# Kernel optimization log

Hardware: AMD Instinct MI355X
Metric: run time of the kernel (lower is better)

## Reference

```python
import jax, jax.numpy as jnp
import numpy as np

L, P = 16384, 512
DT_MIN, DT_MAX = 0.001, 0.1
THRESHOLD = 1.0  # spike threshold assumed for cartesian_spike


def setup_inputs() -> dict:
    key = jax.random.key(0)
    k1, k2, k3, k4, k5, k6 = jax.random.split(key, 6)
    u = jax.random.normal(k1, (L, P), dtype=jnp.float32)
    # Stored Lambda param: [..., 0] = log(-Re(Lambda)) with Re(Lambda) < 0, [..., 1] = Im(Lambda)
    lam_real_neg = jax.random.uniform(k2, (P,), minval=0.1, maxval=1.0)  # -Re(Lambda)
    lam_imag = jax.random.normal(k3, (P,)) * 3.0
    Lambda = jnp.stack([jnp.log(lam_real_neg), lam_imag], axis=-1).astype(jnp.float32)
    # init_log_steps: log(dt) uniform in [log(dt_min), log(dt_max)], shape (P, 1)
    log_step = (np.log(DT_MIN) + jax.random.uniform(k4, (P, 1)) * (np.log(DT_MAX) - np.log(DT_MIN))).astype(jnp.float32)
    V_re = jax.random.normal(k5, (P, P), dtype=jnp.float32) / np.sqrt(P)
    V_im = jax.random.normal(k6, (P, P), dtype=jnp.float32) / np.sqrt(P)
    return {"u": u, "Lambda": Lambda, "log_step": log_step, "V_re": V_re, "V_im": V_im}


def _binop(q_i, q_j):
    A_i, b_i = q_i
    A_j, b_j = q_j
    return (A_j * A_i, A_j * b_i + b_j)


def reference(u, Lambda, log_step, V_re, V_im):
    # keep_imag = False: u stays real. discretization = 'zoh', activation = 'cartesian_spike'.
    Lambda_tilde = -jnp.exp(Lambda[..., 0]) + 1j * Lambda[..., 1]            # (P,) complex
    step = jnp.exp(log_step[:, 0])                                            # (P,)
    Lambda_bar = jnp.exp(Lambda_tilde * step)                                 # (P,) |.|<1
    # B_tilde = I, so zoh gives B_bar = diag((Lambda_bar - 1)/Lambda); B_bar @ u_t = coef * u_t
    B_coef = (Lambda_bar - 1.0) / Lambda_tilde                                # (P,)
    Lambda_elements = jnp.broadcast_to(Lambda_bar, (u.shape[0], Lambda_bar.shape[0]))
    Bu_elements = B_coef[None, :] * u.astype(Lambda_bar.dtype)                # (L, P) complex
    _, xs = jax.lax.associative_scan(_binop, (Lambda_elements, Bu_elements))  # (L, P)
    V = V_re + 1j * V_im
    xs = xs @ V.T                                                             # vmap(V @ x) over L
    spikes = (xs.real > THRESHOLD).astype(jnp.float32)                        # cartesian_spike
    return spikes
```

## Files before the change

### kernel.cpp

```cpp
#include <hip/hip_runtime.h>

#define L_LEN   16384
#define P_DIM   512
#define CHUNK   32
#define NCHUNK  512

#define KDIM    1024
#define NDIM    512
#define BM      128
#define BN      64
#define BK      64

typedef __bf16 bf16_t;
typedef __bf16 bf16x8 __attribute__((ext_vector_type(8)));
typedef float  floatx4 __attribute__((ext_vector_type(4)));

__device__ __forceinline__ uint32_t pack_bf16(float a, float b) {
    bf16_t ha = (bf16_t)a, hb = (bf16_t)b;
    return (uint32_t)__builtin_bit_cast(unsigned short, ha)
         | ((uint32_t)__builtin_bit_cast(unsigned short, hb) << 16);
}

__device__ __forceinline__ void ch_consts(float lam0, float lam1, float ls,
                                          float& ar, float& ai,
                                          float& br, float& bi) {
    float lr = -expf(lam0);
    float li = lam1;
    float s  = expf(ls);
    float er = expf(lr * s);
    ar = er * cosf(li * s);
    ai = er * sinf(li * s);
    float dr = ar - 1.0f, di = ai;
    float inv = 1.0f / (lr * lr + li * li);
    br = (dr * lr + di * li) * inv;
    bi = (di * lr - dr * li) * inv;
}

__global__ void __launch_bounds__(256) k_scan_ends(const float* __restrict__ u,
        const float* __restrict__ Lam, const float* __restrict__ lstep,
        const float* __restrict__ Vre, const float* __restrict__ Vim,
        float2* __restrict__ endv, bf16_t* __restrict__ Bt) {
    const int t = threadIdx.x;
    const int c = blockIdx.x;

    {
        int idx = c * 256 + t;
        float2 vr = ((const float2*)Vre)[idx];
        float2 vi = ((const float2*)Vim)[idx];
        ((uint2*)Bt)[idx] = make_uint2(pack_bf16(vr.x, -vi.x),
                                       pack_bf16(vr.y, -vi.y));
    }

    float4 lam4 = ((const float4*)Lam)[t];
    float2 ls2  = ((const float2*)lstep)[t];
    float ar0, ai0, br0, bi0, ar1, ai1, br1, bi1;
    ch_consts(lam4.x, lam4.y, ls2.x, ar0, ai0, br0, bi0);
    ch_consts(lam4.z, lam4.w, ls2.y, ar1, ai1, br1, bi1);

    float xr0 = 0.f, xi0 = 0.f, xr1 = 0.f, xi1 = 0.f;
    const float2* up = (const float2*)(u + (size_t)c * CHUNK * P_DIM) + t;
    #pragma unroll 8
    for (int k = 0; k < CHUNK; ++k) {
        float2 uv = up[(size_t)k * (P_DIM / 2)];
        float nr0 = ar0 * xr0 - ai0 * xi0 + br0 * uv.x;
        float ni0 = ar0 * xi0 + ai0 * xr0 + bi0 * uv.x;
        float nr1 = ar1 * xr1 - ai1 * xi1 + br1 * uv.y;
        float ni1 = ar1 * xi1 + ai1 * xr1 + bi1 * uv.y;
        xr0 = nr0; xi0 = ni0; xr1 = nr1; xi1 = ni1;
    }
    ((float4*)endv)[c * 256 + t] = make_float4(xr0, xi0, xr1, xi1);
}

__global__ void __launch_bounds__(1024) k_carry(const float* __restrict__ Lam,
        const float* __restrict__ lstep, const float2* __restrict__ endv,
        float2* __restrict__ carry) {
    __shared__ float2 zl[NCHUNK * 2];
    const int tid = threadIdx.x;
    const int g = tid & 1;
    const int c = tid >> 1;
    const int p = blockIdx.x * 2 + g;

    float lr = -expf(Lam[2 * p + 0]);
    float li = Lam[2 * p + 1];
    float s  = expf(lstep[p]);
    float tt = s * (float)CHUNK;
    float er = expf(lr * tt);
    float Ar = er * cosf(li * tt);
    float Ai = er * sinf(li * tt);

    float2 e = endv[(size_t)c * P_DIM + p];
    float zr = e.x, zi = e.y;
    zl[c * 2 + g] = make_float2(zr, zi);
    __syncthreads();
    for (int st = 1; st < NCHUNK; st <<= 1) {
        float tr = 0.f, ti = 0.f;
        if (c >= st) { float2 v = zl[(c - st) * 2 + g]; tr = v.x; ti = v.y; }
        __syncthreads();
        zr += Ar * tr - Ai * ti;
        zi += Ar * ti + Ai * tr;
        zl[c * 2 + g] = make_float2(zr, zi);
        float nAr = Ar * Ar - Ai * Ai;
        float nAi = 2.f * Ar * Ai;
        Ar = nAr; Ai = nAi;
        __syncthreads();
    }
    float2 cv = make_float2(0.f, 0.f);
    if (c > 0) cv = zl[(c - 1) * 2 + g];
    carry[(size_t)c * P_DIM + p] = cv;
}

__global__ void __launch_bounds__(256) k_materialize(const float* __restrict__ u,
        const float* __restrict__ Lam, const float* __restrict__ lstep,
        const float2* __restrict__ carry, bf16_t* __restrict__ A) {
    const int t = threadIdx.x;
    const int c = blockIdx.x;

    float4 lam4 = ((const float4*)Lam)[t];
    float2 ls2  = ((const float2*)lstep)[t];
    float ar0, ai0, br0, bi0, ar1, ai1, br1, bi1;
    ch_consts(lam4.x, lam4.y, ls2.x, ar0, ai0, br0, bi0);
    ch_consts(lam4.z, lam4.w, ls2.y, ar1, ai1, br1, bi1);

    float4 cv = ((const float4*)carry)[c * 256 + t];
    float xr0 = cv.x, xi0 = cv.y, xr1 = cv.z, xi1 = cv.w;
    const float2* up = (const float2*)(u + (size_t)c * CHUNK * P_DIM) + t;
    uint2* Ap = (uint2*)(A + (size_t)c * CHUNK * KDIM) + t;
    #pragma unroll 4
    for (int k = 0; k < CHUNK; ++k) {
        float2 uv = up[(size_t)k * (P_DIM / 2)];
        float nr0 = ar0 * xr0 - ai0 * xi0 + br0 * uv.x;
        float ni0 = ar0 * xi0 + ai0 * xr0 + bi0 * uv.x;
        float nr1 = ar1 * xr1 - ai1 * xi1 + br1 * uv.y;
        float ni1 = ar1 * xi1 + ai1 * xr1 + bi1 * uv.y;
        xr0 = nr0; xi0 = ni0; xr1 = nr1; xi1 = ni1;
        Ap[(size_t)k * 256] = make_uint2(pack_bf16(xr0, xi0),
                                         pack_bf16(xr1, xi1));
    }
}

__global__ void __launch_bounds__(256, 4) k_gemm(const bf16_t* __restrict__ A,
        const bf16_t* __restrict__ Bt, float* __restrict__ out) {
    __shared__ uint4 As4[BM * BK * 2 / 16];
    __shared__ uint4 Bs4[BN * BK * 2 / 16];

    const int tid  = threadIdx.x;
    const int lane = tid & 63;
    const int w    = tid >> 6;
    const int m0   = blockIdx.x * BM;
    const int n0   = blockIdx.y * BN;
    const int wm   = (w >> 1) * 64;
    const int wn   = (w & 1) * 32;

    const int fr_m = lane & 15;
    const int fr_g = lane >> 4;

    floatx4 acc[4][2];
    #pragma unroll
    for (int i = 0; i < 4; ++i)
        #pragma unroll
        for (int j = 0; j < 2; ++j) {
            floatx4 z = {0.f, 0.f, 0.f, 0.f};
            acc[i][j] = z;
        }

    const bf16_t* Asrc = A  + (size_t)m0 * KDIM;
    const bf16_t* Bsrc = Bt + (size_t)n0 * KDIM;

    const bf16_t* ga[4]; char* la[4];
    const bf16_t* gb[2]; char* lb[2];
    #pragma unroll
    for (int i = 0; i < 4; ++i) {
        int q   = i * 256 + tid;
        int row = q >> 3;
        int gc  = (q & 7) ^ (row & 7);
        ga[i] = Asrc + (size_t)row * KDIM + gc * 8;
        la[i] = (char*)As4 + (size_t)q * 16;
    }
    #pragma unroll
    for (int i = 0; i < 2; ++i) {
        int q   = i * 256 + tid;
        int row = q >> 3;
        int gc  = (q & 7) ^ (row & 7);
        gb[i] = Bsrc + (size_t)row * KDIM + gc * 8;
        lb[i] = (char*)Bs4 + (size_t)q * 16;
    }

    for (int kt = 0; kt < KDIM; kt += BK) {
        __syncthreads();
        #pragma unroll
        for (int i = 0; i < 4; ++i)
            __builtin_amdgcn_global_load_lds(
                (const __attribute__((address_space(1))) void*)(ga[i] + kt),
                (__attribute__((address_space(3))) void*)la[i], 16, 0, 0);
        #pragma unroll
        for (int i = 0; i < 2; ++i)
            __builtin_amdgcn_global_load_lds(
                (const __attribute__((address_space(1))) void*)(gb[i] + kt),
                (__attribute__((address_space(3))) void*)lb[i], 16, 0, 0);
        __syncthreads();
        #pragma unroll
        for (int kk = 0; kk < BK; kk += 32) {
            bf16x8 af[4], bf[2];
            #pragma unroll
            for (int i = 0; i < 4; ++i) {
                int m  = wm + i * 16 + fr_m;
                int cc = (kk >> 3) + fr_g;
                int sc = cc ^ (m & 7);
                af[i] = *(const bf16x8*)((const bf16_t*)As4 + m * BK + sc * 8);
            }
            #pragma unroll
            for (int j = 0; j < 2; ++j) {
                int n  = wn + j * 16 + fr_m;
                int cc = (kk >> 3) + fr_g;
                int sc = cc ^ (n & 7);
                bf[j] = *(const bf16x8*)((const bf16_t*)Bs4 + n * BK + sc * 8);
            }
            #pragma unroll
            for (int i = 0; i < 4; ++i)
                #pragma unroll
                for (int j = 0; j < 2; ++j)
                    acc[i][j] = __builtin_amdgcn_mfma_f32_16x16x32_bf16(
                        af[i], bf[j], acc[i][j], 0, 0, 0);
        }
    }

    #pragma unroll
    for (int i = 0; i < 4; ++i)
        #pragma unroll
        for (int j = 0; j < 2; ++j)
            #pragma unroll
            for (int r = 0; r < 4; ++r) {
                int rr = wm + i * 16 + fr_g * 4 + r;
                int cl = wn + j * 16 + fr_m;
                float v = acc[i][j][r];
                out[(size_t)(m0 + rr) * NDIM + (n0 + cl)] = (v > 1.0f) ? 1.0f : 0.0f;
            }
}

extern "C" void kernel_launch(void* const* d_in, const int* in_sizes, int n_in,
                              void* d_out, int out_size, void* d_ws, size_t ws_size,
                              hipStream_t stream) {
    (void)in_sizes; (void)n_in; (void)out_size; (void)ws_size;
    const float* u     = (const float*)d_in[0];
    const float* Lam   = (const float*)d_in[1];
    const float* lstep = (const float*)d_in[2];
    const float* Vre   = (const float*)d_in[3];
    const float* Vim   = (const float*)d_in[4];
    float* out = (float*)d_out;

    char* ws = (char*)d_ws;
    const size_t endv_bytes  = (size_t)NCHUNK * P_DIM * sizeof(float2);
    const size_t carry_bytes = endv_bytes;
    const size_t bt_bytes    = (size_t)NDIM * KDIM * sizeof(bf16_t);
    float2* endv  = (float2*)(ws);
    float2* carry = (float2*)(ws + endv_bytes);
    bf16_t* Bt    = (bf16_t*)(ws + endv_bytes + carry_bytes);
    bf16_t* A     = (bf16_t*)(ws + endv_bytes + carry_bytes + bt_bytes);

    hipLaunchKernelGGL(k_scan_ends, dim3(NCHUNK), dim3(256), 0, stream,
                       u, Lam, lstep, Vre, Vim, endv, Bt);
    hipLaunchKernelGGL(k_carry, dim3(P_DIM / 2), dim3(1024), 0, stream,
                       Lam, lstep, endv, carry);
    hipLaunchKernelGGL(k_materialize, dim3(NCHUNK), dim3(256), 0, stream,
                       u, Lam, lstep, carry, A);
    hipLaunchKernelGGL(k_gemm, dim3(L_LEN / BM, NDIM / BN), dim3(256), 0, stream,
                       A, Bt, out);
}
```

Before: 127.8 us.

## Fuse chunk scan materialization into GEMM, keeping scanned states in LDS

Removes the separate materialize kernel and the bf16 A matrix in global memory. Each block of 512 threads now rescans a 64-row slab (two chunks) from the carry, writes the packed bf16 states into a swizzled 128KB LDS tile, then runs the full-K MFMA GEMM across all 512 output columns. B fragments are read directly from global memory without LDS staging. This saves the A write and read round trip and one launch. In exchange it uses large LDS, which limits occupancy, runs a serial 64-step scan per block, and issues uncoalesced direct global B loads.

```diff
diff --git a/kernel.cpp b/kernel.cpp
--- a/kernel.cpp
+++ b/kernel.cpp
@@ -7,9 +7,8 @@
 
 #define KDIM    1024
 #define NDIM    512
-#define BM      128
-#define BN      64
-#define BK      64
+#define BM      64
+#define NBLK    (L_LEN / BM)
 
 typedef __bf16 bf16_t;
 typedef __bf16 bf16x8 __attribute__((ext_vector_type(8)));
@@ -109,131 +108,86 @@
     carry[(size_t)c * P_DIM + p] = cv;
 }
 
-__global__ void __launch_bounds__(256) k_materialize(const float* __restrict__ u,
+__global__ void __launch_bounds__(512, 2) k_scan_gemm(const float* __restrict__ u,
         const float* __restrict__ Lam, const float* __restrict__ lstep,
-        const float2* __restrict__ carry, bf16_t* __restrict__ A) {
-    const int t = threadIdx.x;
-    const int c = blockIdx.x;
-
-    float4 lam4 = ((const float4*)Lam)[t];
-    float2 ls2  = ((const float2*)lstep)[t];
-    float ar0, ai0, br0, bi0, ar1, ai1, br1, bi1;
-    ch_consts(lam4.x, lam4.y, ls2.x, ar0, ai0, br0, bi0);
-    ch_consts(lam4.z, lam4.w, ls2.y, ar1, ai1, br1, bi1);
-
-    float4 cv = ((const float4*)carry)[c * 256 + t];
-    float xr0 = cv.x, xi0 = cv.y, xr1 = cv.z, xi1 = cv.w;
-    const float2* up = (const float2*)(u + (size_t)c * CHUNK * P_DIM) + t;
-    uint2* Ap = (uint2*)(A + (size_t)c * CHUNK * KDIM) + t;
-    #pragma unroll 4
-    for (int k = 0; k < CHUNK; ++k) {
-        float2 uv = up[(size_t)k * (P_DIM / 2)];
-        float nr0 = ar0 * xr0 - ai0 * xi0 + br0 * uv.x;
-        float ni0 = ar0 * xi0 + ai0 * xr0 + bi0 * uv.x;
-        float nr1 = ar1 * xr1 - ai1 * xi1 + br1 * uv.y;
-        float ni1 = ar1 * xi1 + ai1 * xr1 + bi1 * uv.y;
-        xr0 = nr0; xi0 = ni0; xr1 = nr1; xi1 = ni1;
-        Ap[(size_t)k * 256] = make_uint2(pack_bf16(xr0, xi0),
-                                         pack_bf16(xr1, xi1));
-    }
-}
-
-__global__ void __launch_bounds__(256, 4) k_gemm(const bf16_t* __restrict__ A,
-        const bf16_t* __restrict__ Bt, float* __restrict__ out) {
-    __shared__ uint4 As4[BM * BK * 2 / 16];
-    __shared__ uint4 Bs4[BN * BK * 2 / 16];
-
-    const int tid  = threadIdx.x;
+        const float2* __restrict__ carry, const bf16_t* __restrict__ Bt,
+        float* __restrict__ out) {
+    __shared__ bf16_t As[BM * KDIM];
+
+    const int tid = threadIdx.x;
+    const int c   = blockIdx.x;
+
+    {
+        const int p = tid;
+        float ar, ai, br, bi;
+        ch_consts(Lam[2 * p + 0], Lam[2 * p + 1], lstep[p], ar, ai, br, bi);
+        float2 cv = carry[(size_t)(2 * c) * P_DIM + p];
+        float xr = cv.x, xi = cv.y;
+        const float* up = u + (size_t)c * BM * P_DIM + p;
+        const int ct  = p >> 2;
+        const int sub = (p & 3) * 4;
+        #pragma unroll 4
+        for (int k = 0; k < BM; ++k) {
+            float uv = up[(size_t)k * P_DIM];
+            float nr = ar * xr - ai * xi + br * uv;
+            float ni = ar * xi + ai * xr + bi * uv;
+            xr = nr; xi = ni;
+            int st = ct ^ (k & 7);
+            *(uint32_t*)((char*)As + (size_t)k * 2048 + st * 16 + sub)
+                = pack_bf16(xr, xi);
+        }
+    }
+    __syncthreads();
+
     const int lane = tid & 63;
     const int w    = tid >> 6;
-    const int m0   = blockIdx.x * BM;
-    const int n0   = blockIdx.y * BN;
-    const int wm   = (w >> 1) * 64;
-    const int wn   = (w & 1) * 32;
-
+    const int wn   = w * 64;
     const int fr_m = lane & 15;
     const int fr_g = lane >> 4;
 
-    floatx4 acc[4][2];
+    floatx4 acc[4][4];
     #pragma unroll
     for (int i = 0; i < 4; ++i)
         #pragma unroll
-        for (int j = 0; j < 2; ++j) {
+        for (int j = 0; j < 4; ++j) {
             floatx4 z = {0.f, 0.f, 0.f, 0.f};
             acc[i][j] = z;
         }
 
-    const bf16_t* Asrc = A  + (size_t)m0 * KDIM;
-    const bf16_t* Bsrc = Bt + (size_t)n0 * KDIM;
-
-    const bf16_t* ga[4]; char* la[4];
-    const bf16_t* gb[2]; char* lb[2];
-    #pragma unroll
-    for (int i = 0; i < 4; ++i) {
-        int q   = i * 256 + tid;
-        int row = q >> 3;
-        int gc  = (q & 7) ^ (row & 7);
-        ga[i] = Asrc + (size_t)row * KDIM + gc * 8;
-        la[i] = (char*)As4 + (size_t)q * 16;
-    }
-    #pragma unroll
-    for (int i = 0; i < 2; ++i) {
-        int q   = i * 256 + tid;
-        int row = q >> 3;
-        int gc  = (q & 7) ^ (row & 7);
-        gb[i] = Bsrc + (size_t)row * KDIM + gc * 8;
-        lb[i] = (char*)Bs4 + (size_t)q * 16;
-    }
-
-    for (int kt = 0; kt < KDIM; kt += BK) {
-        __syncthreads();
+    const bf16_t* Bw = Bt + (size_t)(wn + fr_m) * KDIM + fr_g * 8;
+
+    #pragma unroll 2
+    for (int kt = 0; kt < KDIM; kt += 32) {
+        bf16x8 af[4], bf[4];
+        #pragma unroll
+        for (int j = 0; j < 4; ++j)
+            bf[j] = *(const bf16x8*)(Bw + (size_t)j * 16 * KDIM + kt);
+        #pragma unroll
+        for (int i = 0; i < 4; ++i) {
+            int m  = i * 16 + fr_m;
+            int cc = (kt >> 3) + fr_g;
+            int sc = cc ^ (m & 7);
+            af[i] = *(const bf16x8*)((const char*)As + (size_t)m * 2048 + sc * 16);
+        }
         #pragma unroll
         for (int i = 0; i < 4; ++i)
-            __builtin_amdgcn_global_load_lds(
-                (const __attribute__((address_space(1))) void*)(ga[i] + kt),
-                (__attribute__((address_space(3))) void*)la[i], 16, 0, 0);
-        #pragma unroll
-        for (int i = 0; i < 2; ++i)
-            __builtin_amdgcn_global_load_lds(
-                (const __attribute__((address_space(1))) void*)(gb[i] + kt),
-                (__attribute__((address_space(3))) void*)lb[i], 16, 0, 0);
-        __syncthreads();
-        #pragma unroll
-        for (int kk = 0; kk < BK; kk += 32) {
-            bf16x8 af[4], bf[2];
             #pragma unroll
-            for (int i = 0; i < 4; ++i) {
-                int m  = wm + i * 16 + fr_m;
-                int cc = (kk >> 3) + fr_g;
-                int sc = cc ^ (m & 7);
-                af[i] = *(const bf16x8*)((const bf16_t*)As4 + m * BK + sc * 8);
-            }
-            #pragma unroll
-            for (int j = 0; j < 2; ++j) {
-                int n  = wn + j * 16 + fr_m;
-                int cc = (kk >> 3) + fr_g;
-                int sc = cc ^ (n & 7);
-                bf[j] = *(const bf16x8*)((const bf16_t*)Bs4 + n * BK + sc * 8);
-            }
-            #pragma unroll
-            for (int i = 0; i < 4; ++i)
-                #pragma unroll
-                for (int j = 0; j < 2; ++j)
-                    acc[i][j] = __builtin_amdgcn_mfma_f32_16x16x32_bf16(
-                        af[i], bf[j], acc[i][j], 0, 0, 0);
-        }
-    }
-
+            for (int j = 0; j < 4; ++j)
+                acc[i][j] = __builtin_amdgcn_mfma_f32_16x16x32_bf16(
+                    af[i], bf[j], acc[i][j], 0, 0, 0);
+    }
+
+    float* outb = out + (size_t)c * BM * NDIM;
     #pragma unroll
     for (int i = 0; i < 4; ++i)
         #pragma unroll
-        for (int j = 0; j < 2; ++j)
+        for (int j = 0; j < 4; ++j)
             #pragma unroll
             for (int r = 0; r < 4; ++r) {
-                int rr = wm + i * 16 + fr_g * 4 + r;
+                int rr = i * 16 + fr_g * 4 + r;
                 int cl = wn + j * 16 + fr_m;
                 float v = acc[i][j][r];
-                out[(size_t)(m0 + rr) * NDIM + (n0 + cl)] = (v > 1.0f) ? 1.0f : 0.0f;
+                outb[(size_t)rr * NDIM + cl] = (v > 1.0f) ? 1.0f : 0.0f;
             }
 }
 
@@ -251,18 +205,14 @@
     char* ws = (char*)d_ws;
     const size_t endv_bytes  = (size_t)NCHUNK * P_DIM * sizeof(float2);
     const size_t carry_bytes = endv_bytes;
-    const size_t bt_bytes    = (size_t)NDIM * KDIM * sizeof(bf16_t);
     float2* endv  = (float2*)(ws);
     float2* carry = (float2*)(ws + endv_bytes);
     bf16_t* Bt    = (bf16_t*)(ws + endv_bytes + carry_bytes);
-    bf16_t* A     = (bf16_t*)(ws + endv_bytes + carry_bytes + bt_bytes);
 
     hipLaunchKernelGGL(k_scan_ends, dim3(NCHUNK), dim3(256), 0, stream,
                        u, Lam, lstep, Vre, Vim, endv, Bt);
     hipLaunchKernelGGL(k_carry, dim3(P_DIM / 2), dim3(1024), 0, stream,
                        Lam, lstep, endv, carry);
-    hipLaunchKernelGGL(k_materialize, dim3(NCHUNK), dim3(256), 0, stream,
-                       u, Lam, lstep, carry, A);
-    hipLaunchKernelGGL(k_gemm, dim3(L_LEN / BM, NDIM / BN), dim3(256), 0, stream,
-                       A, Bt, out);
-}
+    hipLaunchKernelGGL(k_scan_gemm, dim3(NBLK), dim3(512), 0, stream,
+                       u, Lam, lstep, carry, Bt, out);
+}
```

Measured after the change: 135.8 us. 1.06x slower.

## Double-buffer GEMM LDS tiles to overlap global loads with MFMA

Applied to the files above, without the earlier changes.

Doubles the shared-memory A and B tiles so the next K-slice is fetched into the alternate buffer with global_load_lds while the current slice feeds MFMA. This replaces two barriers per iteration with one and aims to hide global-load latency. The larger LDS footprint lowers the launch-bounds occupancy hint from 4 to 3 blocks. The loads are asynchronous, and correctness depends on the single barrier both waiting for the prefetch and ordering buffer reuse.

```diff
diff --git a/kernel.cpp b/kernel.cpp
--- a/kernel.cpp
+++ b/kernel.cpp
@@ -138,10 +138,10 @@
     }
 }
 
-__global__ void __launch_bounds__(256, 4) k_gemm(const bf16_t* __restrict__ A,
+__global__ void __launch_bounds__(256, 3) k_gemm(const bf16_t* __restrict__ A,
         const bf16_t* __restrict__ Bt, float* __restrict__ out) {
-    __shared__ uint4 As4[BM * BK * 2 / 16];
-    __shared__ uint4 Bs4[BN * BK * 2 / 16];
+    __shared__ uint4 As4[2 * BM * BK * 2 / 16];
+    __shared__ uint4 Bs4[2 * BN * BK * 2 / 16];
 
     const int tid  = threadIdx.x;
     const int lane = tid & 63;
@@ -185,43 +185,64 @@
         lb[i] = (char*)Bs4 + (size_t)q * 16;
     }
 
+    #pragma unroll
+    for (int i = 0; i < 4; ++i)
+        __builtin_amdgcn_global_load_lds(
+            (const __attribute__((address_space(1))) void*)(ga[i]),
+            (__attribute__((address_space(3))) void*)(la[i]), 16, 0, 0);
+    #pragma unroll
+    for (int i = 0; i < 2; ++i)
+        __builtin_amdgcn_global_load_lds(
+            (const __attribute__((address_space(1))) void*)(gb[i]),
+            (__attribute__((address_space(3))) void*)(lb[i]), 16, 0, 0);
+    __syncthreads();
+
+    int cur = 0;
+    #pragma unroll
     for (int kt = 0; kt < KDIM; kt += BK) {
-        __syncthreads();
-        #pragma unroll
-        for (int i = 0; i < 4; ++i)
-            __builtin_amdgcn_global_load_lds(
-                (const __attribute__((address_space(1))) void*)(ga[i] + kt),
-                (__attribute__((address_space(3))) void*)la[i], 16, 0, 0);
-        #pragma unroll
-        for (int i = 0; i < 2; ++i)
-            __builtin_amdgcn_global_load_lds(
-                (const __attribute__((address_space(1))) void*)(gb[i] + kt),
-                (__attribute__((address_space(3))) void*)lb[i], 16, 0, 0);
-        __syncthreads();
+        if (kt + BK < KDIM) {
+            const int nxt = cur ^ 1;
+            #pragma unroll
+            for (int i = 0; i < 4; ++i)
+                __builtin_amdgcn_global_load_lds(
+                    (const __attribute__((address_space(1))) void*)(ga[i] + kt + BK),
+                    (__attribute__((address_space(3))) void*)(la[i] + nxt * 16384),
+                    16, 0, 0);
+            #pragma unroll
+            for (int i = 0; i < 2; ++i)
+                __builtin_amdgcn_global_load_lds(
+                    (const __attribute__((address_space(1))) void*)(gb[i] + kt + BK),
+                    (__attribute__((address_space(3))) void*)(lb[i] + nxt * 8192),
+                    16, 0, 0);
+        }
+        const bf16_t* Abase = (const bf16_t*)As4 + cur * (BM * BK);
+        const bf16_t* Bbase = (const bf16_t*)Bs4 + cur * (BN * BK);
         #pragma unroll
         for (int kk = 0; kk < BK; kk += 32) {
-            bf16x8 af[4], bf[2];
+            bf16x8 af[4], bfv[2];
             #pragma unroll
             for (int i = 0; i < 4; ++i) {
                 int m  = wm + i * 16 + fr_m;
                 int cc = (kk >> 3) + fr_g;
                 int sc = cc ^ (m & 7);
-                af[i] = *(const bf16x8*)((const bf16_t*)As4 + m * BK + sc * 8);
+                af[i] = *(const bf16x8*)(Abase + m * BK + sc * 8);
             }
             #pragma unroll
             for (int j = 0; j < 2; ++j) {
                 int n  = wn + j * 16 + fr_m;
                 int cc = (kk >> 3) + fr_g;
                 int sc = cc ^ (n & 7);
-                bf[j] = *(const bf16x8*)((const bf16_t*)Bs4 + n * BK + sc * 8);
+                bfv[j] = *(const bf16x8*)(Bbase + n * BK + sc * 8);
             }
             #pragma unroll
             for (int i = 0; i < 4; ++i)
                 #pragma unroll
                 for (int j = 0; j < 2; ++j)
                     acc[i][j] = __builtin_amdgcn_mfma_f32_16x16x32_bf16(
-                        af[i], bf[j], acc[i][j], 0, 0, 0);
+                        af[i], bfv[j], acc[i][j], 0, 0, 0);
         }
+        __syncthreads();
+        cur ^= 1;
     }
 
     #pragma unroll
```

Measured after the change: 139.2 us. 1.09x slower.

## Double-buffer GEMM LDS tiles to overlap global loads with MFMA compute

Applied to the files above, without the earlier changes.

The bf16 GEMM k-loop now keeps two LDS stages for the A and B tiles. It issues async global_load_lds for the tile two steps ahead while MFMAs consume the current one, using s_waitcnt vmcnt(6) plus raw barriers in place of two __syncthreads per iteration. The goal is to hide global-memory latency behind compute. In exchange, LDS per block doubles to 48KB and launch bounds drop from 4 to 3 blocks per CU, which reduces occupancy.

```diff
diff --git a/kernel.cpp b/kernel.cpp
--- a/kernel.cpp
+++ b/kernel.cpp
@@ -138,10 +138,10 @@
     }
 }
 
-__global__ void __launch_bounds__(256, 4) k_gemm(const bf16_t* __restrict__ A,
+__global__ void __launch_bounds__(256, 3) k_gemm(const bf16_t* __restrict__ A,
         const bf16_t* __restrict__ Bt, float* __restrict__ out) {
-    __shared__ uint4 As4[BM * BK * 2 / 16];
-    __shared__ uint4 Bs4[BN * BK * 2 / 16];
+    __shared__ uint4 As4[2 * BM * BK * 2 / 16];
+    __shared__ uint4 Bs4[2 * BN * BK * 2 / 16];
 
     const int tid  = threadIdx.x;
     const int lane = tid & 63;
@@ -185,44 +185,71 @@
         lb[i] = (char*)Bs4 + (size_t)q * 16;
     }
 
-    for (int kt = 0; kt < KDIM; kt += BK) {
-        __syncthreads();
-        #pragma unroll
-        for (int i = 0; i < 4; ++i)
-            __builtin_amdgcn_global_load_lds(
-                (const __attribute__((address_space(1))) void*)(ga[i] + kt),
-                (__attribute__((address_space(3))) void*)la[i], 16, 0, 0);
-        #pragma unroll
-        for (int i = 0; i < 2; ++i)
-            __builtin_amdgcn_global_load_lds(
-                (const __attribute__((address_space(1))) void*)(gb[i] + kt),
-                (__attribute__((address_space(3))) void*)lb[i], 16, 0, 0);
-        __syncthreads();
-        #pragma unroll
-        for (int kk = 0; kk < BK; kk += 32) {
-            bf16x8 af[4], bf[2];
-            #pragma unroll
-            for (int i = 0; i < 4; ++i) {
-                int m  = wm + i * 16 + fr_m;
-                int cc = (kk >> 3) + fr_g;
-                int sc = cc ^ (m & 7);
-                af[i] = *(const bf16x8*)((const bf16_t*)As4 + m * BK + sc * 8);
-            }
-            #pragma unroll
-            for (int j = 0; j < 2; ++j) {
-                int n  = wn + j * 16 + fr_m;
-                int cc = (kk >> 3) + fr_g;
-                int sc = cc ^ (n & 7);
-                bf[j] = *(const bf16x8*)((const bf16_t*)Bs4 + n * BK + sc * 8);
-            }
-            #pragma unroll
-            for (int i = 0; i < 4; ++i)
-                #pragma unroll
-                for (int j = 0; j < 2; ++j)
-                    acc[i][j] = __builtin_amdgcn_mfma_f32_16x16x32_bf16(
-                        af[i], bf[j], acc[i][j], 0, 0, 0);
-        }
-    }
+#define STAGE(KT, BUF)                                                        \
+    do {                                                                      \
+        _Pragma("unroll")                                                     \
+        for (int i_ = 0; i_ < 4; ++i_)                                        \
+            __builtin_amdgcn_global_load_lds(                                 \
+                (const __attribute__((address_space(1))) void*)(ga[i_] + (KT)),\
+                (__attribute__((address_space(3))) void*)(la[i_] + (BUF) * 16384),\
+                16, 0, 0);                                                    \
+        _Pragma("unroll")                                                     \
+        for (int i_ = 0; i_ < 2; ++i_)                                        \
+            __builtin_amdgcn_global_load_lds(                                 \
+                (const __attribute__((address_space(1))) void*)(gb[i_] + (KT)),\
+                (__attribute__((address_space(3))) void*)(lb[i_] + (BUF) * 8192),\
+                16, 0, 0);                                                    \
+    } while (0)
+
+#define COMPUTE(BUF)                                                          \
+    do {                                                                      \
+        const bf16_t* Abase = (const bf16_t*)As4 + (BUF) * (BM * BK);         \
+        const bf16_t* Bbase = (const bf16_t*)Bs4 + (BUF) * (BN * BK);         \
+        _Pragma("unroll")                                                     \
+        for (int kk = 0; kk < BK; kk += 32) {                                 \
+            bf16x8 af[4], bfv[2];                                             \
+            _Pragma("unroll")                                                 \
+            for (int i_ = 0; i_ < 4; ++i_) {                                  \
+                int m  = wm + i_ * 16 + fr_m;                                 \
+                int cc = (kk >> 3) + fr_g;                                    \
+                int sc = cc ^ (m & 7);                                        \
+                af[i_] = *(const bf16x8*)(Abase + m * BK + sc * 8);           \
+            }                                                                 \
+            _Pragma("unroll")                                                 \
+            for (int j_ = 0; j_ < 2; ++j_) {                                  \
+                int n  = wn + j_ * 16 + fr_m;                                 \
+                int cc = (kk >> 3) + fr_g;                                    \
+                int sc = cc ^ (n & 7);                                        \
+                bfv[j_] = *(const bf16x8*)(Bbase + n * BK + sc * 8);          \
+            }                                                                 \
+            _Pragma("unroll")                                                 \
+            for (int i_ = 0; i_ < 4; ++i_)                                    \
+                _Pragma("unroll")                                             \
+                for (int j_ = 0; j_ < 2; ++j_)                                \
+                    acc[i_][j_] = __builtin_amdgcn_mfma_f32_16x16x32_bf16(    \
+                        af[i_], bfv[j_], acc[i_][j_], 0, 0, 0);               \
+        }                                                                     \
+    } while (0)
+
+    STAGE(0, 0);
+    STAGE(BK, 1);
+
+    int cur = 0;
+    for (int kt = 0; kt < KDIM - BK; kt += BK) {
+        asm volatile("s_waitcnt vmcnt(6)" ::: "memory");
+        __builtin_amdgcn_s_barrier();
+        COMPUTE(cur);
+        __builtin_amdgcn_s_barrier();
+        if (kt + 2 * BK < KDIM)
+            STAGE(kt + 2 * BK, cur);
+        cur ^= 1;
+    }
+    asm volatile("s_waitcnt vmcnt(0)" ::: "memory");
+    __builtin_amdgcn_s_barrier();
+    COMPUTE(cur);
+
+#undef STAGE
+#undef COMPUTE
 
     #pragma unroll
     for (int i = 0; i < 4; ++i)
```

After: 134.5 us. 1.05x slower.
